# Optimization experiments

Measured on AMD Instinct MI355X. Metric: run time of the kernel, lower is better.

Reference implementation:

```python
import jax, jax.numpy as jnp
import numpy as np

D = 1024  # input_size == context_size
B, SQ, SKV = 4, 2048, 2048


def setup_inputs() -> dict:
    key = jax.random.key(0)
    ks = jax.random.split(key, 8)
    s = 1.0 / np.sqrt(D)
    return {
        "x": jax.random.normal(ks[0], (B, SQ, D), jnp.float32),
        "context": jax.random.normal(ks[1], (B, SKV, D), jnp.float32),
        "Wq": jax.random.uniform(ks[2], (D, D), jnp.float32, -s, s),
        "bq": jnp.zeros((D,), jnp.float32),
        "Wk": jax.random.uniform(ks[3], (D, D), jnp.float32, -s, s),
        "bk": jnp.zeros((D,), jnp.float32),
        "Wv": jax.random.uniform(ks[4], (D, D), jnp.float32, -s, s),
        "bv": jnp.zeros((D,), jnp.float32),
    }


def reference(x, context, Wq, bq, Wk, bk, Wv, bv):
    # Linear layers (torch nn.Linear: y = x @ W^T + b; here W stored as [in, out])
    Q = x @ Wq + bq                  # [B, SQ, D]
    K = context @ Wk + bk            # [B, SKV, D]
    V = context @ Wv + bv            # [B, SKV, D]
    scale = 1.0 / np.sqrt(D).astype(np.float32)
    scores = jnp.einsum("bqd,bkd->bqk", Q, K) * scale  # [B, SQ, SKV]
    attn = jax.nn.softmax(scores, axis=-1)
    out = jnp.einsum("bqk,bkd->bqd", attn, V)          # [B, SQ, D]
    return out
```

## Files before the change

kernel.cpp:

```cpp
#include <hip/hip_runtime.h>
#include <cstdint>
#include <cstddef>

typedef __attribute__((ext_vector_type(8))) short short8;
typedef __attribute__((ext_vector_type(16))) float floatx16;

__device__ __forceinline__ unsigned short f2bf(float f) {
    union { float f; unsigned int u; } v; v.f = f;
    unsigned int r = v.u + 0x7fffu + ((v.u >> 16) & 1u);
    return (unsigned short)(r >> 16);
}

__device__ __forceinline__ void glds16(const void* g, void* l) {
    __builtin_amdgcn_global_load_lds(
        (const __attribute__((address_space(1))) void*)g,
        (__attribute__((address_space(3))) void*)l, 16, 0, 0);
}

#define EPI_ROW(r, kg) (((r) & 3) + 8 * ((r) >> 2) + 4 * (kg))

__device__ __forceinline__ void gemm_core(
    const unsigned short* __restrict__ Ab, int ldA,
    const unsigned short* __restrict__ Bb, int ldB,
    int K,
    unsigned short* __restrict__ As, unsigned short* __restrict__ Bs,
    floatx16 (&acc)[2][2])
{
    const int tid = threadIdx.x;
    const int wave = tid >> 6, lane = tid & 63;

    const unsigned short* gA[4];
    const unsigned short* gB[4];
#pragma unroll
    for (int i = 0; i < 4; ++i) {
        const int c = i * 256 + tid;
        const int row = c >> 3;
        const int l = (c & 7) ^ ((row ^ (row >> 3)) & 7);
        gA[i] = Ab + (size_t)row * ldA + l * 8;
        gB[i] = Bb + (size_t)row * ldB + l * 8;
    }
    const int arow = (wave >> 1) * 64 + (lane & 31);
    const int brow = (wave & 1) * 64 + (lane & 31);
    const int kg = lane >> 5;
    const int sw = (lane & 7) ^ ((lane >> 3) & 3);
    const unsigned short* pa = As + arow * 64;
    const unsigned short* pb = Bs + brow * 64;

    for (int k0 = 0; k0 < K; k0 += 64) {
#pragma unroll
        for (int i = 0; i < 4; ++i)
            glds16(gA[i] + k0, As + (size_t)(i * 256 + wave * 64) * 8);
#pragma unroll
        for (int i = 0; i < 4; ++i)
            glds16(gB[i] + k0, Bs + (size_t)(i * 256 + wave * 64) * 8);
        __syncthreads();
#pragma unroll
        for (int s = 0; s < 4; ++s) {
            const int o0 = ((2 * s + kg) ^ sw) * 8;
            const int o1 = o0 ^ 32;
            short8 a0 = *(const short8*)(pa + o0);
            short8 a1 = *(const short8*)(pa + 32 * 64 + o1);
            short8 b0 = *(const short8*)(pb + o0);
            short8 b1 = *(const short8*)(pb + 32 * 64 + o1);
            acc[0][0] = __builtin_amdgcn_mfma_f32_32x32x16_bf16(a0, b0, acc[0][0], 0, 0, 0);
            acc[0][1] = __builtin_amdgcn_mfma_f32_32x32x16_bf16(a0, b1, acc[0][1], 0, 0, 0);
            acc[1][0] = __builtin_amdgcn_mfma_f32_32x32x16_bf16(a1, b0, acc[1][0], 0, 0, 0);
            acc[1][1] = __builtin_amdgcn_mfma_f32_32x32x16_bf16(a1, b1, acc[1][1], 0, 0, 0);
        }
        __syncthreads();
    }
}

__device__ __forceinline__ void gemm256_core(
    const unsigned short* __restrict__ Ab, int ldA,
    const unsigned short* __restrict__ Bb, int ldB,
    int K,
    unsigned short* __restrict__ As, unsigned short* __restrict__ Bs,
    floatx16 (&acc)[4][2])
{
    const int tid = threadIdx.x;
    const int wave = tid >> 6, lane = tid & 63;
    const int wm = wave >> 2, wn = wave & 3;
    const int kg = lane >> 5;
    const int l31 = lane & 31;
    const int NT = K >> 6;

    const int grow = tid >> 3;
    const int gsl = (tid & 7) ^ ((grow ^ (grow >> 3)) & 7);
    const unsigned short* gA = Ab + (size_t)grow * ldA + gsl * 8;
    const unsigned short* gB = Bb + (size_t)grow * ldB + gsl * 8;
    unsigned short* dA = As + wave * 512;
    unsigned short* dB = Bs + wave * 512;

#define STG_A(t, h) do { if ((t) < NT) { \
    const unsigned short* s_ = gA + (size_t)(h) * 128 * ldA + (t) * 64; \
    unsigned short* d_ = dA + ((((t) & 1) << 1) + (h)) * 8192; \
    glds16(s_, d_); glds16(s_ + (size_t)64 * ldA, d_ + 4096); } } while (0)
#define STG_B(t, h) do { if ((t) < NT) { \
    const unsigned short* s_ = gB + (size_t)(h) * 128 * ldB + (t) * 64; \
    unsigned short* d_ = dB + ((((t) & 1) << 1) + (h)) * 8192; \
    glds16(s_, d_); glds16(s_ + (size_t)64 * ldB, d_ + 4096); } } while (0)

    const int sw = (lane & 7) ^ ((lane >> 3) & 3);
    const int swB = sw ^ ((wn & 1) << 2);
    const int paoff = (wm * 64 + l31) * 64;
    const int pboff = (wn * 32 + l31) * 64;

    STG_A(0, 0); STG_B(0, 0); STG_B(0, 1); STG_A(0, 1);
    STG_A(1, 0); STG_B(1, 0); STG_B(1, 1);
    asm volatile("s_waitcnt vmcnt(8)" ::: "memory");
    __builtin_amdgcn_s_barrier();

    short8 a0[4], a1[4], b0[4], b1[4];
    for (int t = 0; t < NT; ++t) {
        const unsigned short* pa = As + ((t & 1) << 1) * 8192 + paoff;
        const unsigned short* pb = Bs + ((t & 1) << 1) * 8192 + pboff;

#pragma unroll
        for (int s = 0; s < 4; ++s) {
            const int oa = ((2 * s + kg) ^ sw) * 8;
            const int ob = ((2 * s + kg) ^ swB) * 8;
            a0[s] = *(const short8*)(pa + oa);
            a1[s] = *(const short8*)(pa + 2048 + (oa ^ 32));
            b0[s] = *(const short8*)(pb + ob);
        }
        STG_A(t + 1, 1);
        __builtin_amdgcn_s_barrier();
        __builtin_amdgcn_s_setprio(1);
#pragma unroll
        for (int s = 0; s < 4; ++s) {
            acc[0][0] = __builtin_amdgcn_mfma_f32_32x32x16_bf16(a0[s], b0[s], acc[0][0], 0, 0, 0);
            acc[0][1] = __builtin_amdgcn_mfma_f32_32x32x16_bf16(a1[s], b0[s], acc[0][1], 0, 0, 0);
        }
        __builtin_amdgcn_s_setprio(0);
        __builtin_amdgcn_s_barrier();

#pragma unroll
        for (int s = 0; s < 4; ++s) {
            const int ob = ((2 * s + kg) ^ swB) * 8;
            b1[s] = *(const short8*)(pb + 8192 + ob);
        }
        STG_A(t + 2, 0);
        __builtin_amdgcn_s_barrier();
        __builtin_amdgcn_s_setprio(1);
#pragma unroll
        for (int s = 0; s < 4; ++s) {
            acc[1][0] = __builtin_amdgcn_mfma_f32_32x32x16_bf16(a0[s], b1[s], acc[1][0], 0, 0, 0);
            acc[1][1] = __builtin_amdgcn_mfma_f32_32x32x16_bf16(a1[s], b1[s], acc[1][1], 0, 0, 0);
        }
        __builtin_amdgcn_s_setprio(0);
        if (t + 2 < NT)      { asm volatile("s_waitcnt vmcnt(10)" ::: "memory"); }
        else if (t + 1 < NT) { asm volatile("s_waitcnt vmcnt(8)"  ::: "memory"); }
        else                 { asm volatile("s_waitcnt vmcnt(0)"  ::: "memory"); }
        __builtin_amdgcn_s_barrier();

#pragma unroll
        for (int s = 0; s < 4; ++s) {
            const int oa = ((2 * s + kg) ^ sw) * 8;
            a0[s] = *(const short8*)(pa + 8192 + oa);
            a1[s] = *(const short8*)(pa + 8192 + 2048 + (oa ^ 32));
        }
        STG_B(t + 2, 0);
        __builtin_amdgcn_s_barrier();
        __builtin_amdgcn_s_setprio(1);
#pragma unroll
        for (int s = 0; s < 4; ++s) {
            acc[2][0] = __builtin_amdgcn_mfma_f32_32x32x16_bf16(a0[s], b1[s], acc[2][0], 0, 0, 0);
            acc[2][1] = __builtin_amdgcn_mfma_f32_32x32x16_bf16(a1[s], b1[s], acc[2][1], 0, 0, 0);
        }
        __builtin_amdgcn_s_setprio(0);
        __builtin_amdgcn_s_barrier();

        STG_B(t + 2, 1);
        __builtin_amdgcn_s_barrier();
        __builtin_amdgcn_s_setprio(1);
#pragma unroll
        for (int s = 0; s < 4; ++s) {
            acc[3][0] = __builtin_amdgcn_mfma_f32_32x32x16_bf16(a0[s], b0[s], acc[3][0], 0, 0, 0);
            acc[3][1] = __builtin_amdgcn_mfma_f32_32x32x16_bf16(a1[s], b0[s], acc[3][1], 0, 0, 0);
        }
        __builtin_amdgcn_s_setprio(0);
        if (t + 2 < NT)      { asm volatile("s_waitcnt vmcnt(8)" ::: "memory"); }
        else if (t + 1 < NT) { asm volatile("s_waitcnt vmcnt(2)" ::: "memory"); }
        else                 { asm volatile("s_waitcnt vmcnt(0)" ::: "memory"); }
        __builtin_amdgcn_s_barrier();
    }
#undef STG_A
#undef STG_B
}

__global__ __launch_bounds__(256) void prep_kernel(
    const float* __restrict__ x, const float* __restrict__ ctx,
    const float* __restrict__ Wq, const float* __restrict__ Wk, const float* __restrict__ Wv,
    unsigned short* __restrict__ xb, unsigned short* __restrict__ cb,
    unsigned short* __restrict__ Wt0, unsigned short* __restrict__ WtKV) {
    const int b = blockIdx.x;
    if (b < 16384) {
        int i = b * 256 + threadIdx.x;
        const float* in; unsigned short* out; int j;
        if (i < 2097152) { in = x; out = xb; j = i; }
        else { in = ctx; out = cb; j = i - 2097152; }
        float4 v = reinterpret_cast<const float4*>(in)[j];
        ushort4 o;
        o.x = f2bf(v.x); o.y = f2bf(v.y); o.z = f2bf(v.z); o.w = f2bf(v.w);
        reinterpret_cast<ushort4*>(out)[j] = o;
    } else {
        __shared__ float tile[32][33];
        const int z = b - 16384;
        const int w = z >> 10, t = z & 1023;
        const float* in = (w == 0) ? Wq : (w == 1) ? Wk : Wv;
        unsigned short* out = (w == 0) ? Wt0 : (w == 1) ? WtKV : (WtKV + 1024 * 1024);
        const int c0 = (t & 31) * 32, r0 = (t >> 5) * 32;
        const int tx = threadIdx.x & 31, ty = threadIdx.x >> 5;
#pragma unroll
        for (int j = 0; j < 4; ++j)
            tile[ty + j * 8][tx] = in[(size_t)(r0 + ty + j * 8) * 1024 + c0 + tx];
        __syncthreads();
#pragma unroll
        for (int j = 0; j < 4; ++j)
            out[(size_t)(c0 + ty + j * 8) * 1024 + r0 + tx] = f2bf(tile[tx][ty + j * 8]);
    }
}

__global__ __launch_bounds__(512, 2) void qkv_kernel(
    const unsigned short* __restrict__ xb, const unsigned short* __restrict__ cb,
    const unsigned short* __restrict__ WtQ, const unsigned short* __restrict__ WtKV,
    const float* __restrict__ bq, const float* __restrict__ bk, const float* __restrict__ bv,
    unsigned short* __restrict__ Qb, unsigned short* __restrict__ Kb,
    unsigned short* __restrict__ Vt) {
    __shared__ unsigned short As[32768];
    __shared__ unsigned short Bs[32768];
    const int bi = blockIdx.x;
    const int i = (bi & 7) * 48 + (bi >> 3);
    const bool isQ = i < 128;
    int by, bx;
    const unsigned short *A, *B;
    if (isQ) {
        by = i >> 2; bx = i & 3;
        A = xb + (size_t)by * 256 * 1024;
        B = WtQ + (size_t)bx * 256 * 1024;
    } else {
        const int j = i - 128;
        by = j >> 3; bx = j & 7;
        A = cb + (size_t)by * 256 * 1024;
        B = WtKV + (size_t)bx * 256 * 1024;
    }
    floatx16 acc[4][2];
#pragma unroll
    for (int q = 0; q < 4; ++q)
#pragma unroll
        for (int h = 0; h < 2; ++h)
#pragma unroll
            for (int r = 0; r < 16; ++r) acc[q][h][r] = 0.f;

    gemm256_core(A, 1024, B, 1024, 1024, As, Bs, acc);

    const int tid = threadIdx.x;
    const int wave = tid >> 6, lane = tid & 63;
    const int wm = wave >> 2, wn = wave & 3;
    const int kg = lane >> 5, l31 = lane & 31;
    const int rowbase = by * 256 + wm * 64;
    const int colbase = bx * 256 + wn * 32 + l31;
#pragma unroll
    for (int q = 0; q < 4; ++q) {
        const int qm = q >> 1;
        const int qn = (q >> 1) ^ (q & 1);
        const int col = colbase + qn * 128;
        const bool isV = (!isQ) && (bx * 256 + qn * 128 >= 1024);
        if (!isV) {
            unsigned short* O = isQ ? Qb : Kb;
            const float bvv = isQ ? bq[col] : bk[col];
#pragma unroll
            for (int mt = 0; mt < 2; ++mt)
#pragma unroll
                for (int r = 0; r < 16; ++r) {
                    const int row = rowbase + qm * 128 + mt * 32 + EPI_ROW(r, kg);
                    O[(size_t)row * 1024 + col] = f2bf(acc[q][mt][r] + bvv);
                }
        } else {
            const int colv = col - 1024;
            const float bvv = bv[colv];
#pragma unroll
            for (int mt = 0; mt < 2; ++mt) {
                const int rowg = rowbase + qm * 128 + mt * 32 + 4 * kg;
                const int bb = rowg >> 11, qb = rowg & 2047;
#pragma unroll
                for (int g = 0; g < 4; ++g) {
                    ushort4 u;
                    u.x = f2bf(acc[q][mt][g * 4 + 0] + bvv);
                    u.y = f2bf(acc[q][mt][g * 4 + 1] + bvv);
                    u.z = f2bf(acc[q][mt][g * 4 + 2] + bvv);
                    u.w = f2bf(acc[q][mt][g * 4 + 3] + bvv);
                    *reinterpret_cast<ushort4*>(Vt + (size_t)bb * 2097152 + (size_t)colv * 2048 + qb + 8 * g) = u;
                }
            }
        }
    }
}

__global__ __launch_bounds__(512, 2) void qkt_kernel(
    const unsigned short* __restrict__ Qb, const unsigned short* __restrict__ Kb,
    unsigned short* __restrict__ Sb, float* __restrict__ l) {
    __shared__ unsigned short As[32768];
    __shared__ unsigned short Bs[32768];
    const int bi = blockIdx.x;
    const int i = (bi & 7) * 32 + (bi >> 3);
    const int z = i >> 6, j = i & 63;
    const int by = j >> 3, bx = j & 7;
    const unsigned short* A = Qb + (size_t)z * 2097152 + (size_t)by * 256 * 1024;
    const unsigned short* B = Kb + (size_t)z * 2097152 + (size_t)bx * 256 * 1024;
    floatx16 acc[4][2];
#pragma unroll
    for (int q = 0; q < 4; ++q)
#pragma unroll
        for (int h = 0; h < 2; ++h)
#pragma unroll
            for (int r = 0; r < 16; ++r) acc[q][h][r] = 0.f;

    gemm256_core(A, 1024, B, 1024, 1024, As, Bs, acc);

    const int tid = threadIdx.x;
    const int wave = tid >> 6, lane = tid & 63;
    const int wm = wave >> 2, wn = wave & 3;
    const int kg = lane >> 5, l31 = lane & 31;
    unsigned short* C = Sb + (size_t)z * 4194304;
    float* lz = l + z * 2048;
    const int rowbase = by * 256 + wm * 64;
    const int colbase = bx * 256 + wn * 32 + l31;
#pragma unroll
    for (int h = 0; h < 2; ++h) {
        const int qA = h ? 3 : 0;
        const int qB = h ? 2 : 1;
#pragma unroll
        for (int mt = 0; mt < 2; ++mt)
#pragma unroll
            for (int r = 0; r < 16; ++r) {
                const int row = rowbase + h * 128 + mt * 32 + EPI_ROW(r, kg);
                const float e0 = __expf(acc[qA][mt][r] * 0.03125f);
                const float e1 = __expf(acc[qB][mt][r] * 0.03125f);
                C[(size_t)row * 2048 + colbase] = f2bf(e0);
                C[(size_t)row * 2048 + colbase + 128] = f2bf(e1);
                float s = e0 + e1;
                s += __shfl_xor(s, 1);  s += __shfl_xor(s, 2);
                s += __shfl_xor(s, 4);  s += __shfl_xor(s, 8);
                s += __shfl_xor(s, 16);
                if (l31 == mt * 16 + r) atomicAdd(&lz[row], s);
            }
    }
}

__global__ __launch_bounds__(256, 4) void pv_kernel(
    const unsigned short* __restrict__ Sb, const unsigned short* __restrict__ Vt,
    const float* __restrict__ l, float* __restrict__ out) {
    __shared__ unsigned short As[128 * 64];
    __shared__ unsigned short Bs[128 * 64];
    const int i = blockIdx.x;
    const int z = (i >> 1) & 3;
    const int slot = i >> 3;
    const int by = (i & 1) + 2 * (slot & 7);
    const int bx = slot >> 3;
    const unsigned short* A = Sb + (size_t)z * 4194304 + (size_t)by * 128 * 2048;
    const unsigned short* B = Vt + (size_t)z * 2097152 + (size_t)bx * 128 * 2048;
    floatx16 acc[2][2];
#pragma unroll
    for (int a = 0; a < 2; ++a)
#pragma unroll
        for (int bj = 0; bj < 2; ++bj)
#pragma unroll
            for (int r = 0; r < 16; ++r) acc[a][bj][r] = 0.f;

    gemm_core(A, 2048, B, 2048, 2048, As, Bs, acc);

    const int wave = threadIdx.x >> 6, lane = threadIdx.x & 63;
    const int kg = lane >> 5;
    float* C = out + (size_t)z * 2097152;
    const float* lz = l + z * 2048;
    const int cm = by * 128 + (wave >> 1) * 64;
    const int cn = bx * 128 + (wave & 1) * 64 + (lane & 31);
#pragma unroll
    for (int mt = 0; mt < 2; ++mt)
#pragma unroll
        for (int r = 0; r < 16; ++r) {
            const int row = cm + mt * 32 + EPI_ROW(r, kg);
            const float inv = 1.0f / lz[row];
            C[(size_t)row * 1024 + cn] = acc[mt][0][r] * inv;
            C[(size_t)row * 1024 + cn + 32] = acc[mt][1][r] * inv;
        }
}

extern "C" void kernel_launch(void* const* d_in, const int* in_sizes, int n_in,
                              void* d_out, int out_size, void* d_ws, size_t ws_size,
                              hipStream_t stream) {
    const float* x   = (const float*)d_in[0];
    const float* ctx = (const float*)d_in[1];
    const float* Wq  = (const float*)d_in[2];
    const float* bq  = (const float*)d_in[3];
    const float* Wk  = (const float*)d_in[4];
    const float* bk  = (const float*)d_in[5];
    const float* Wv  = (const float*)d_in[6];
    const float* bv  = (const float*)d_in[7];
    float* out = (float*)d_out;

    const size_t MB = 1024 * 1024;
    char* ws = (char*)d_ws;
    unsigned short* xb   = (unsigned short*)(ws + 0 * MB);
    unsigned short* cb   = (unsigned short*)(ws + 16 * MB);
    unsigned short* Qb   = (unsigned short*)(ws + 32 * MB);
    unsigned short* Kb   = (unsigned short*)(ws + 48 * MB);
    unsigned short* Vt   = (unsigned short*)(ws + 64 * MB);
    unsigned short* Wt0  = (unsigned short*)(ws + 80 * MB);
    unsigned short* WtKV = (unsigned short*)(ws + 82 * MB);
    unsigned short* Sb   = (unsigned short*)(ws + 86 * MB);
    float*          lrow = (float*)(ws + 118 * MB);

    hipMemsetAsync(lrow, 0, 8192 * sizeof(float), stream);
    prep_kernel<<<16384 + 3072, 256, 0, stream>>>(x, ctx, Wq, Wk, Wv, xb, cb, Wt0, WtKV);
    qkv_kernel<<<384, 512, 0, stream>>>(xb, cb, Wt0, WtKV, bq, bk, bv, Qb, Kb, Vt);
    qkt_kernel<<<256, 512, 0, stream>>>(Qb, Kb, Sb, lrow);
    pv_kernel<<<512, 256, 0, stream>>>(Sb, Vt, lrow, out);
}
```

Before: 291.2 us.

## Split QKV projection into separate KV and Q kernels, fold memset into prep

```diff
diff --git a/kernel.cpp b/kernel.cpp
--- a/kernel.cpp
+++ b/kernel.cpp
@@ -193,7 +193,8 @@
     const float* __restrict__ x, const float* __restrict__ ctx,
     const float* __restrict__ Wq, const float* __restrict__ Wk, const float* __restrict__ Wv,
     unsigned short* __restrict__ xb, unsigned short* __restrict__ cb,
-    unsigned short* __restrict__ Wt0, unsigned short* __restrict__ WtKV) {
+    unsigned short* __restrict__ Wt0, unsigned short* __restrict__ WtKV,
+    float* __restrict__ lrow) {
     const int b = blockIdx.x;
     if (b < 16384) {
         int i = b * 256 + threadIdx.x;
@@ -204,7 +205,7 @@
         ushort4 o;
         o.x = f2bf(v.x); o.y = f2bf(v.y); o.z = f2bf(v.z); o.w = f2bf(v.w);
         reinterpret_cast<ushort4*>(out)[j] = o;
-    } else {
+    } else if (b < 19456) {
         __shared__ float tile[32][33];
         const int z = b - 16384;
         const int w = z >> 10, t = z & 1023;
@@ -219,32 +220,23 @@
 #pragma unroll
         for (int j = 0; j < 4; ++j)
             out[(size_t)(c0 + ty + j * 8) * 1024 + r0 + tx] = f2bf(tile[tx][ty + j * 8]);
-    }
-}
-
-__global__ __launch_bounds__(512, 2) void qkv_kernel(
-    const unsigned short* __restrict__ xb, const unsigned short* __restrict__ cb,
-    const unsigned short* __restrict__ WtQ, const unsigned short* __restrict__ WtKV,
-    const float* __restrict__ bq, const float* __restrict__ bk, const float* __restrict__ bv,
-    unsigned short* __restrict__ Qb, unsigned short* __restrict__ Kb,
-    unsigned short* __restrict__ Vt) {
+    } else {
+        const int i = (b - 19456) * 256 + threadIdx.x;
+        reinterpret_cast<float4*>(lrow)[i] = float4{0.f, 0.f, 0.f, 0.f};
+    }
+}
+
+__global__ __launch_bounds__(512, 2) void qkv_kv_kernel(
+    const unsigned short* __restrict__ cb, const unsigned short* __restrict__ WtKV,
+    const float* __restrict__ bk, const float* __restrict__ bv,
+    unsigned short* __restrict__ Kb, unsigned short* __restrict__ Vt) {
     __shared__ unsigned short As[32768];
     __shared__ unsigned short Bs[32768];
     const int bi = blockIdx.x;
-    const int i = (bi & 7) * 48 + (bi >> 3);
-    const bool isQ = i < 128;
-    int by, bx;
-    const unsigned short *A, *B;
-    if (isQ) {
-        by = i >> 2; bx = i & 3;
-        A = xb + (size_t)by * 256 * 1024;
-        B = WtQ + (size_t)bx * 256 * 1024;
-    } else {
-        const int j = i - 128;
-        by = j >> 3; bx = j & 7;
-        A = cb + (size_t)by * 256 * 1024;
-        B = WtKV + (size_t)bx * 256 * 1024;
-    }
+    const int i = (bi & 7) * 32 + (bi >> 3);
+    const int by = i >> 3, bx = i & 7;
+    const unsigned short* A = cb + (size_t)by * 256 * 1024;
+    const unsigned short* B = WtKV + (size_t)bx * 256 * 1024;
     floatx16 acc[4][2];
 #pragma unroll
     for (int q = 0; q < 4; ++q)
@@ -266,16 +258,14 @@
         const int qm = q >> 1;
         const int qn = (q >> 1) ^ (q & 1);
         const int col = colbase + qn * 128;
-        const bool isV = (!isQ) && (bx * 256 + qn * 128 >= 1024);
-        if (!isV) {
-            unsigned short* O = isQ ? Qb : Kb;
-            const float bvv = isQ ? bq[col] : bk[col];
+        if (bx * 256 + qn * 128 < 1024) {
+            const float bvv = bk[col];
 #pragma unroll
             for (int mt = 0; mt < 2; ++mt)
 #pragma unroll
                 for (int r = 0; r < 16; ++r) {
                     const int row = rowbase + qm * 128 + mt * 32 + EPI_ROW(r, kg);
-                    O[(size_t)row * 1024 + col] = f2bf(acc[q][mt][r] + bvv);
+                    Kb[(size_t)row * 1024 + col] = f2bf(acc[q][mt][r] + bvv);
                 }
         } else {
             const int colv = col - 1024;
@@ -295,6 +285,45 @@
                 }
             }
         }
+    }
+}
+
+__global__ __launch_bounds__(256, 4) void qkv_q_kernel(
+    const unsigned short* __restrict__ xb, const unsigned short* __restrict__ WtQ,
+    const float* __restrict__ bq, unsigned short* __restrict__ Qb) {
+    __shared__ unsigned short As[128 * 64];
+    __shared__ unsigned short Bs[128 * 64];
+    const int i = blockIdx.x;
+    const int slot = i >> 3;
+    const int by = (i & 7) + 8 * (slot & 7);
+    const int bx = slot >> 3;
+    const unsigned short* A = xb + (size_t)by * 128 * 1024;
+    const unsigned short* B = WtQ + (size_t)bx * 128 * 1024;
+    floatx16 acc[2][2];
+#pragma unroll
+    for (int a = 0; a < 2; ++a)
+#pragma unroll
+        for (int bj = 0; bj < 2; ++bj)
+#pragma unroll
+            for (int r = 0; r < 16; ++r) acc[a][bj][r] = 0.f;
+
+    gemm_core(A, 1024, B, 1024, 1024, As, Bs, acc);
+
+    const int wave = threadIdx.x >> 6, lane = threadIdx.x & 63;
+    const int kg = lane >> 5;
+    const int cm = by * 128 + (wave >> 1) * 64;
+    const int cn = bx * 128 + (wave & 1) * 64 + (lane & 31);
+#pragma unroll
+    for (int nt = 0; nt < 2; ++nt) {
+        const int col = cn + nt * 32;
+        const float bvv = bq[col];
+#pragma unroll
+        for (int mt = 0; mt < 2; ++mt)
+#pragma unroll
+            for (int r = 0; r < 16; ++r) {
+                const int row = cm + mt * 32 + EPI_ROW(r, kg);
+                Qb[(size_t)row * 1024 + col] = f2bf(acc[mt][nt][r] + bvv);
+            }
     }
 }
 
@@ -413,9 +442,9 @@
     unsigned short* Sb   = (unsigned short*)(ws + 86 * MB);
     float*          lrow = (float*)(ws + 118 * MB);
 
-    hipMemsetAsync(lrow, 0, 8192 * sizeof(float), stream);
-    prep_kernel<<<16384 + 3072, 256, 0, stream>>>(x, ctx, Wq, Wk, Wv, xb, cb, Wt0, WtKV);
-    qkv_kernel<<<384, 512, 0, stream>>>(xb, cb, Wt0, WtKV, bq, bk, bv, Qb, Kb, Vt);
+    prep_kernel<<<16384 + 3072 + 8, 256, 0, stream>>>(x, ctx, Wq, Wk, Wv, xb, cb, Wt0, WtKV, lrow);
+    qkv_kv_kernel<<<256, 512, 0, stream>>>(cb, WtKV, bk, bv, Kb, Vt);
+    qkv_q_kernel<<<512, 256, 0, stream>>>(xb, Wt0, bq, Qb);
     qkt_kernel<<<256, 512, 0, stream>>>(Qb, Kb, Sb, lrow);
     pv_kernel<<<512, 256, 0, stream>>>(Sb, Vt, lrow, out);
 }
```

Result: no change. 285.9 us (-1.8%).
